# Kernel tuning notes

Hardware: AMD Instinct MI355X
Metric: run time of the kernel (lower is better)

## Reference

```python
import math
import jax, jax.numpy as jnp
import numpy as np

H = 4  # num heads
D = 512
MLP = 1024
EPS = 1e-6


def _ln(x, g, b):
    m = x.mean(-1, keepdims=True)
    v = ((x - m) ** 2).mean(-1, keepdims=True)
    return (x - m) / jnp.sqrt(v + EPS) * g + b


def _heads(x):
    B, S, d = x.shape
    return x.reshape(B, S, H, d // H).transpose(0, 2, 1, 3)  # [B,H,S,hd]


def _att(q, k, v, Wo, bo):
    # q,k,v: [B,S,D] already projected
    hd = q.shape[-1] // H
    qh, kh, vh = _heads(q), _heads(k), _heads(v)
    scores = jnp.einsum('bhqd,bhkd->bhqk', qh, kh) / math.sqrt(hd)
    probs = jax.nn.softmax(scores, axis=-1)
    ctx = jnp.einsum('bhqk,bhkd->bhqd', probs, vh)
    B, _, S, _ = ctx.shape
    ctx = ctx.transpose(0, 2, 1, 3).reshape(B, S, H * hd)
    return ctx @ Wo + bo


def setup_inputs() -> dict:
    key = jax.random.key(0)
    ks = jax.random.split(key, 32)
    i = iter(range(32))
    def w(shape, scale=0.02):
        return jax.random.normal(ks[next(i)], shape, dtype=jnp.float32) * scale
    inp = {
        'x1': jax.random.normal(ks[next(i)], (16, 1024, D), dtype=jnp.float32),
        'x2': jax.random.normal(ks[next(i)], (16, 1024, D), dtype=jnp.float32),
        'ln1_g': jnp.ones((D,), jnp.float32), 'ln1_b': jnp.zeros((D,), jnp.float32),
        'ln2_g': jnp.ones((D,), jnp.float32), 'ln2_b': jnp.zeros((D,), jnp.float32),
        'lnf_g': jnp.ones((D,), jnp.float32), 'lnf_b': jnp.zeros((D,), jnp.float32),
    }
    for name in ['q1', 'k1', 'v1', 'q2', 'k2', 'v2', 'q12', 'k12', 'v12', 'o']:
        inp['W' + name] = w((D, D))
        inp['b' + name] = jnp.zeros((D,), jnp.float32)
    inp['W1'] = w((D, MLP)); inp['b1'] = jnp.zeros((MLP,), jnp.float32)
    inp['W2'] = w((MLP, D)); inp['b2'] = jnp.zeros((D,), jnp.float32)
    return inp


def reference(x1, x2, ln1_g, ln1_b, ln2_g, ln2_b, lnf_g, lnf_b,
              Wq1, bq1, Wk1, bk1, Wv1, bv1,
              Wq2, bq2, Wk2, bk2, Wv2, bv2,
              Wq12, bq12, Wk12, bk12, Wv12, bv12,
              Wo, bo, W1, b1, W2, b2):
    identity = x1
    x1n = _ln(x1, ln1_g, ln1_b)
    x2n = _ln(x2, ln2_g, ln2_b)
    # stream-1 self-attention with residual onto normalized input
    src1 = x1n + _att(x1n @ Wq1 + bq1, x1n @ Wk1 + bk1, x1n @ Wv1 + bv1, Wo, bo)
    # stream-2 self-attention
    src2 = x2n + _att(x2n @ Wq2 + bq2, x2n @ Wk2 + bk2, x2n @ Wv2 + bv2, Wo, bo)
    # cross attention: query from src1, key/value from src2
    attn_out = _att(src1 @ Wq12 + bq12, src2 @ Wk12 + bk12, src2 @ Wv12 + bv12, Wo, bo)
    x = attn_out + identity
    h = _ln(x, lnf_g, lnf_b)
    h = jax.nn.gelu(h @ W1 + b1, approximate=False) @ W2 + b2
    return x + h
```

## Files before the change

### kernel.cpp

```cpp
#include <hip/hip_runtime.h>
#include <math.h>


#define SEQ   1024
#define DM    512
#define HDIM  128
#define MTOK  16384
#define MLPD  1024
#define SC2   ((float)(0.08838834764831845 * 1.4426950408889634))

typedef short bf16x8 __attribute__((ext_vector_type(8)));
typedef float f32x4  __attribute__((ext_vector_type(4)));
typedef float f32x16 __attribute__((ext_vector_type(16)));
typedef unsigned short us4 __attribute__((ext_vector_type(4)));

typedef unsigned int u32g __attribute__((address_space(1)));
typedef unsigned int u32l __attribute__((address_space(3)));

static __device__ __forceinline__ unsigned short f2b(float f) {
  union { float f; unsigned u; } v; v.f = f;
  unsigned r = v.u + 0x7FFFu + ((v.u >> 16) & 1u);
  return (unsigned short)(r >> 16);
}
static __device__ __forceinline__ float b2f(unsigned short h) {
  union { unsigned u; float f; } v; v.u = ((unsigned)h) << 16;
  return v.f;
}
static __device__ __forceinline__ unsigned pk2t(float a, float b) {
  union { float f; unsigned u; } va, vb; va.f = a; vb.f = b;
  return __builtin_amdgcn_perm(vb.u, va.u, 0x07060302u);
}
static __device__ __forceinline__ float ex2(float x) {
  float r; asm("v_exp_f32 %0, %1" : "=v"(r) : "v"(x)); return r;
}
static __device__ __forceinline__ void gl_lds16(const void* g, void* l) {
  __builtin_amdgcn_global_load_lds((u32g*)g, (u32l*)l, 16, 0, 0);
}

struct P12 { const float* p[12]; };
struct P9  { const float* p[9]; };

__global__ __launch_bounds__(256) void prep_kernel(P12 ws, P9 bs,
                                                   unsigned short* __restrict__ WT0,
                                                   unsigned short* __restrict__ W1t,
                                                   unsigned short* __restrict__ W2t,
                                                   float* __restrict__ bcc) {
  int bid = blockIdx.x;
  if (bid >= 3584) {
    int i = (bid - 3584) * 256 + threadIdx.x;
    if (i < 4608) bcc[i] = bs.p[i >> 9][i & 511];
    return;
  }
  __shared__ float t[32][33];
  const float* W; unsigned short* Wt; int K, N, tt;
  if (bid < 2560)      { int wi = bid >> 8; W = ws.p[wi]; Wt = WT0 + (size_t)wi * 262144; K = 512; N = 512; tt = bid & 255; }
  else if (bid < 3072) { W = ws.p[10]; Wt = W1t; K = 512;  N = 1024; tt = bid - 2560; }
  else                 { W = ws.p[11]; Wt = W2t; K = 1024; N = 512;  tt = bid - 3072; }
  int ntiles = N >> 5;
  int bx = tt % ntiles, by = tt / ntiles;
  int n0 = bx * 32, k0 = by * 32;
  int tx = threadIdx.x & 31, ty = threadIdx.x >> 5;
#pragma unroll
  for (int i = 0; i < 32; i += 8)
    t[ty + i][tx] = W[(size_t)(k0 + ty + i) * N + n0 + tx];
  __syncthreads();
#pragma unroll
  for (int i = 0; i < 32; i += 8)
    Wt[(size_t)(n0 + ty + i) * K + k0 + tx] = f2b(t[tx][ty + i]);
}

__global__ __launch_bounds__(256) void ln_kernel(const float* __restrict__ X0,
                                                 const float* __restrict__ X1,
                                                 const float* __restrict__ g0w,
                                                 const float* __restrict__ b0w,
                                                 const float* __restrict__ g1w,
                                                 const float* __restrict__ b1w,
                                                 unsigned short* __restrict__ out0,
                                                 unsigned short* __restrict__ out1) {
  int idx  = blockIdx.x * 4 + (threadIdx.x >> 6);
  int sel  = idx >> 14;
  int row  = idx & 16383;
  const float* X = sel ? X1 : X0;
  const float* gw = sel ? g1w : g0w;
  const float* bw = sel ? b1w : b0w;
  unsigned short* outB = sel ? out1 : out0;
  int lane = threadIdx.x & 63;
  const float4* xr = (const float4*)(X + (size_t)row * DM);
  float4 a = xr[lane];
  float4 c = xr[lane + 64];
  float s  = a.x + a.y + a.z + a.w + c.x + c.y + c.z + c.w;
  float s2 = a.x*a.x + a.y*a.y + a.z*a.z + a.w*a.w
           + c.x*c.x + c.y*c.y + c.z*c.z + c.w*c.w;
#pragma unroll
  for (int off = 1; off < 64; off <<= 1) {
    s  += __shfl_xor(s,  off, 64);
    s2 += __shfl_xor(s2, off, 64);
  }
  float mean = s * (1.0f / 512.0f);
  float var  = s2 * (1.0f / 512.0f) - mean * mean;
  float rstd = rsqrtf(var + 1e-6f);
  const float4* gv = (const float4*)gw;
  const float4* bv = (const float4*)bw;
  float4 g1 = gv[lane], g2 = gv[lane + 64];
  float4 b1 = bv[lane], b2 = bv[lane + 64];
  us4 o1, o2;
  o1.x = f2b((a.x - mean) * rstd * g1.x + b1.x);
  o1.y = f2b((a.y - mean) * rstd * g1.y + b1.y);
  o1.z = f2b((a.z - mean) * rstd * g1.z + b1.z);
  o1.w = f2b((a.w - mean) * rstd * g1.w + b1.w);
  o2.x = f2b((c.x - mean) * rstd * g2.x + b2.x);
  o2.y = f2b((c.y - mean) * rstd * g2.y + b2.y);
  o2.z = f2b((c.z - mean) * rstd * g2.z + b2.z);
  o2.w = f2b((c.w - mean) * rstd * g2.w + b2.w);
  *(us4*)(outB + (size_t)row * DM + lane * 4)        = o1;
  *(us4*)(outB + (size_t)row * DM + (lane + 64) * 4) = o2;
}

template <int RES, bool GELU_ACT, int OMODE>
__global__ __launch_bounds__(256, 2) void gemm_kernel(const unsigned short* __restrict__ A,
                                                      const unsigned short* __restrict__ A1,
                                                      const unsigned short* __restrict__ Bt,
                                                      const float* __restrict__ bias,
                                                      const void* __restrict__ res,
                                                      float* __restrict__ outF,
                                                      unsigned short* __restrict__ outB,
                                                      unsigned short* __restrict__ outV,
                                                      int M, int N, int K) {
  int nT = N >> 7;
  int mT = M >> 7;
  int xcd = blockIdx.x & 7;
  int idx = blockIdx.x >> 3;
  int mPerX = mT >> 3;
  int q = idx / nT;
  int tm = xcd * mPerX + q;
  int tn = idx - q * nT;
  int m0 = tm << 7, n0 = tn << 7;
  int tid = threadIdx.x, lane = tid & 63, w = tid >> 6;
  int m16 = lane & 15, q4 = lane >> 4;
  int wr = (w & 1) << 6, wc = (w >> 1) << 6;
  __shared__ unsigned short Alds[2][128 * 64];
  __shared__ unsigned short Blds[2][128 * 64];
  f32x4 acc[4][4] = {};

  const unsigned short* Aeff = A;
  const unsigned short* Bteff = Bt;
  const float* biaseff = bias;
  if (OMODE == 3) {
    int half = tm >> 7;
    Bteff = Bt + (size_t)half * 3 * 262144;
    biaseff = bias + half * 1536;
  }
  if (OMODE == 4) {
    if (tn >= 4) Aeff = A1;
  }

  int srow = lane >> 3;
  int scol = ((lane & 7) ^ srow) << 3;
  const unsigned short* Ag = Aeff  + (size_t)(m0 + w * 8 + srow) * K + scol;
  const unsigned short* Bg = Bteff + (size_t)(n0 + w * 8 + srow) * K + scol;
  int ldst = w * 512;

#pragma unroll
  for (int it = 0; it < 4; ++it) {
    gl_lds16(Ag + (size_t)it * 32 * K, Alds[0] + it * 2048 + ldst);
    gl_lds16(Bg + (size_t)it * 32 * K, Blds[0] + it * 2048 + ldst);
  }

  int nk = K >> 6;
  for (int ks = 0; ks < nk; ++ks) {
    int cur = ks & 1, nxt = cur ^ 1;
    __syncthreads();
    if (ks + 1 < nk) {
      int k0n = (ks + 1) << 6;
#pragma unroll
      for (int it = 0; it < 4; ++it) {
        gl_lds16(Ag + (size_t)it * 32 * K + k0n, Alds[nxt] + it * 2048 + ldst);
        gl_lds16(Bg + (size_t)it * 32 * K + k0n, Blds[nxt] + it * 2048 + ldst);
      }
    }
    const unsigned short* Ar = Alds[cur];
    const unsigned short* Br = Blds[cur];
#pragma unroll
    for (int kk = 0; kk < 64; kk += 32) {
      bf16x8 af[4], bfr[4];
#pragma unroll
      for (int i = 0; i < 4; ++i) {
        int row = wr + i * 16 + m16;
        af[i] = *(const bf16x8*)(Ar + row * 64 + ((((kk >> 3) + q4) ^ (m16 & 7)) << 3));
      }
#pragma unroll
      for (int j = 0; j < 4; ++j) {
        int row = wc + j * 16 + m16;
        bfr[j] = *(const bf16x8*)(Br + row * 64 + ((((kk >> 3) + q4) ^ (m16 & 7)) << 3));
      }
#pragma unroll
      for (int i = 0; i < 4; ++i)
#pragma unroll
        for (int j = 0; j < 4; ++j)
          acc[i][j] = __builtin_amdgcn_mfma_f32_16x16x32_bf16(af[i], bfr[j], acc[i][j], 0, 0, 0);
    }
  }
  if (OMODE == 3 || OMODE == 4) {
    if (n0 < 1024) {
      int stride = (OMODE == 3) ? 1024 : 512;
      unsigned short* ob = outB;
      int coff = 0;
      if (OMODE == 4 && n0 >= 512) { ob = outB + (size_t)MTOK * 512; coff = 512; }
      float sc = (n0 < 512) ? SC2 : 1.0f;
#pragma unroll
      for (int i = 0; i < 4; ++i) {
#pragma unroll
        for (int r = 0; r < 4; ++r) {
          int row = m0 + wr + i * 16 + q4 * 4 + r;
#pragma unroll
          for (int j = 0; j < 4; ++j) {
            int col = n0 + wc + j * 16 + m16;
            ob[(size_t)row * stride + col - coff] = f2b((acc[i][j][r] + biaseff[col]) * sc);
          }
        }
      }
    } else {
#pragma unroll
      for (int i = 0; i < 4; ++i) {
        int row0 = m0 + wr + i * 16 + q4 * 4;
        int s = row0 & 1023, bl = row0 >> 10;
        s = (s & ~12) | ((s & 4) << 1) | ((s & 8) >> 1);
#pragma unroll
        for (int j = 0; j < 4; ++j) {
          int col = n0 + wc + j * 16 + m16;
          int hh = (col - 1024) >> 7, hd = col & 127;
          float bb = biaseff[col];
          us4 pkv;
          pkv.x = f2b(acc[i][j][0] + bb);
          pkv.y = f2b(acc[i][j][1] + bb);
          pkv.z = f2b(acc[i][j][2] + bb);
          pkv.w = f2b(acc[i][j][3] + bb);
          *(us4*)(outV + (((size_t)(bl * 4 + hh)) * HDIM + hd) * SEQ + s) = pkv;
        }
      }
    }
  } else {
#pragma unroll
    for (int i = 0; i < 4; ++i) {
#pragma unroll
      for (int r = 0; r < 4; ++r) {
        int row = m0 + wr + i * 16 + q4 * 4 + r;
#pragma unroll
        for (int j = 0; j < 4; ++j) {
          int col = n0 + wc + j * 16 + m16;
          float v = acc[i][j][r] + bias[col];
          if (RES == 1) v += ((const float*)res)[(size_t)row * N + col];
          if (RES == 2) v += b2f(((const unsigned short*)res)[(size_t)row * N + col]);
          if (GELU_ACT) v = 0.5f * v * (1.0f + erff(v * 0.70710678118654752f));
          if (OMODE == 1) outF[(size_t)row * N + col] = v;
          else            outB[(size_t)row * N + col] = f2b(v);
        }
      }
    }
  }
}

__global__ __launch_bounds__(256, 2) void attn_kernel(const unsigned short* __restrict__ Qb_,
                                                      const unsigned short* __restrict__ Kb_,
                                                      int tstride,
                                                      const unsigned short* __restrict__ Vt,
                                                      unsigned short* __restrict__ CTX,
                                                      int pairs_per_xcd) {
  int xcd = blockIdx.x & 7;
  int i   = blockIdx.x >> 3;
  int pair = xcd * pairs_per_xcd + (i >> 3);
  int qt   = i & 7;
  int b = pair >> 2, h = pair & 3;
  int tid = threadIdx.x, lane = tid & 63, w = tid >> 6;
  int m32 = lane & 31, hf = lane >> 5;
  size_t qkoff = ((size_t)b * SEQ) * tstride + h * HDIM;
  const unsigned short* Qg = Qb_ + qkoff;
  const unsigned short* Kg = Kb_ + qkoff;
  const unsigned short* Vp = Vt + (size_t)pair * HDIM * SEQ;

  __shared__ unsigned short Klds[2][64 * 128];
  __shared__ unsigned short Vlds[2][128 * 64];

  int qrow0 = qt * 128 + w * 32;
  bf16x8 qf[8];
  {
    const unsigned short* qp = Qg + (size_t)(qrow0 + m32) * tstride + hf * 8;
#pragma unroll
    for (int ks = 0; ks < 8; ++ks) qf[ks] = *(const bf16x8*)(qp + ks * 16);
  }
  bf16x8 onesf;
#pragma unroll
  for (int j = 0; j < 8; ++j) onesf[j] = (short)0x3F80;

  const unsigned short* kp0 = Kg + (size_t)(16 * w + (lane >> 4)) * tstride
                              + (((lane & 15) ^ (lane >> 4)) << 3);
  const unsigned short* kp1 = Kg + (size_t)(16 * w + 4 + (lane >> 4)) * tstride
                              + (((lane & 15) ^ ((lane >> 4) + 4)) << 3);
  const unsigned short* vp0 = Vp + (size_t)(32 * w + (lane >> 3)) * SEQ
                              + (((lane & 7) ^ (lane >> 3)) << 3);
  int klo = 16 * w * 128;
  int vlo = 32 * w * 64;

  auto stage = [&](unsigned short* Kb, unsigned short* Vb) {
    gl_lds16(kp0,               Kb + klo);
    gl_lds16(kp1,               Kb + klo + 4 * 128);
    gl_lds16(kp0 + 8 * tstride, Kb + klo + 8 * 128);
    gl_lds16(kp1 + 8 * tstride, Kb + klo + 12 * 128);
    gl_lds16(vp0,               Vb + vlo);
    gl_lds16(vp0 + 8 * SEQ,     Vb + vlo + 8 * 64);
    gl_lds16(vp0 + 16 * SEQ,    Vb + vlo + 16 * 64);
    gl_lds16(vp0 + 24 * SEQ,    Vb + vlo + 24 * 64);
  };
  auto adv = [&]() { kp0 += 64 * tstride; kp1 += 64 * tstride; vp0 += 64; };

  f32x16 o0 = {}, o1 = {}, o2 = {}, o3 = {};
  f32x16 lacc = {};
  bf16x8 pa0, pa1, pa2, pa3;
  bf16x8 pb0, pb1, pb2, pb3;

  auto qk = [&](const unsigned short* Kr, f32x16& s0, f32x16& s1) {
#pragma unroll
    for (int ks = 0; ks < 8; ++ks) {
      int ch = 2 * ks + hf;
      bf16x8 kf0 = *(const bf16x8*)(Kr + m32 * 128 + ((ch ^ (m32 & 7)) << 3));
      s0 = __builtin_amdgcn_mfma_f32_32x32x16_bf16(kf0, qf[ks], s0, 0, 0, 0);
      int k1r = 32 + m32;
      bf16x8 kf1 = *(const bf16x8*)(Kr + k1r * 128 + ((ch ^ (k1r & 7)) << 3));
      s1 = __builtin_amdgcn_mfma_f32_32x32x16_bf16(kf1, qf[ks], s1, 0, 0, 0);
    }
  };
  auto mkpa = [&](const f32x16& s0, const f32x16& s1,
                  bf16x8& q0, bf16x8& q1, bf16x8& q2, bf16x8& q3) {
    union { unsigned u[4]; bf16x8 v; } uu;
#pragma unroll
    for (int g = 0; g < 2; ++g) {
      uu.u[0] = pk2t(ex2(s0[8*g+0]), ex2(s0[8*g+1]));
      uu.u[1] = pk2t(ex2(s0[8*g+2]), ex2(s0[8*g+3]));
      uu.u[2] = pk2t(ex2(s0[8*g+4]), ex2(s0[8*g+5]));
      uu.u[3] = pk2t(ex2(s0[8*g+6]), ex2(s0[8*g+7]));
      if (g == 0) q0 = uu.v; else q1 = uu.v;
    }
#pragma unroll
    for (int g = 0; g < 2; ++g) {
      uu.u[0] = pk2t(ex2(s1[8*g+0]), ex2(s1[8*g+1]));
      uu.u[1] = pk2t(ex2(s1[8*g+2]), ex2(s1[8*g+3]));
      uu.u[2] = pk2t(ex2(s1[8*g+4]), ex2(s1[8*g+5]));
      uu.u[3] = pk2t(ex2(s1[8*g+6]), ex2(s1[8*g+7]));
      if (g == 0) q2 = uu.v; else q3 = uu.v;
    }
  };
  auto pv = [&](const unsigned short* Vr,
                const bf16x8& q0, const bf16x8& q1, const bf16x8& q2, const bf16x8& q3) {
#pragma unroll
    for (int ks = 0; ks < 4; ++ks) {
      const bf16x8& pk = (ks == 0) ? q0 : (ks == 1) ? q1 : (ks == 2) ? q2 : q3;
      int ch = 2 * ks + hf;
      int sw = m32 & 7;
      lacc = __builtin_amdgcn_mfma_f32_32x32x16_bf16(pk, onesf, lacc, 0, 0, 0);
      {
        bf16x8 vf = *(const bf16x8*)(Vr + m32 * 64 + ((ch ^ sw) << 3));
        o0 = __builtin_amdgcn_mfma_f32_32x32x16_bf16(pk, vf, o0, 0, 0, 0);
      }
      {
        bf16x8 vf = *(const bf16x8*)(Vr + (32 + m32) * 64 + ((ch ^ sw) << 3));
        o1 = __builtin_amdgcn_mfma_f32_32x32x16_bf16(pk, vf, o1, 0, 0, 0);
      }
      {
        bf16x8 vf = *(const bf16x8*)(Vr + (64 + m32) * 64 + ((ch ^ sw) << 3));
        o2 = __builtin_amdgcn_mfma_f32_32x32x16_bf16(pk, vf, o2, 0, 0, 0);
      }
      {
        bf16x8 vf = *(const bf16x8*)(Vr + (96 + m32) * 64 + ((ch ^ sw) << 3));
        o3 = __builtin_amdgcn_mfma_f32_32x32x16_bf16(pk, vf, o3, 0, 0, 0);
      }
    }
  };

  stage(Klds[0], Vlds[0]);
  __syncthreads();
  adv();
  stage(Klds[1], Vlds[1]);
  {
    f32x16 s0 = {}, s1 = {};
    qk(Klds[0], s0, s1);
    mkpa(s0, s1, pa0, pa1, pa2, pa3);
  }

  for (int t = 0; t < 15; ++t) {
    int cur = t & 1, nxt = cur ^ 1;
    __syncthreads();
    f32x16 s0 = {}, s1 = {};
    qk(Klds[nxt], s0, s1);
    pv(Vlds[cur], pa0, pa1, pa2, pa3);
    mkpa(s0, s1, pb0, pb1, pb2, pb3);
    __syncthreads();
    if (t < 14) { adv(); stage(Klds[cur], Vlds[cur]); }
    pa0 = pb0; pa1 = pb1; pa2 = pb2; pa3 = pb3;
  }
  pv(Vlds[1], pa0, pa1, pa2, pa3);

  size_t obase = ((size_t)b * SEQ + qrow0) * DM + h * HDIM;
#pragma unroll
  for (int g = 0; g < 4; ++g) {
#pragma unroll
    for (int r = 0; r < 4; ++r) {
      int reg = 4 * g + r;
      int rowl = 8 * g + 4 * hf + r;
      float inv = 1.0f / lacc[reg];
      size_t off = obase + (size_t)rowl * DM + m32;
      CTX[off]      = f2b(o0[reg] * inv);
      CTX[off + 32] = f2b(o1[reg] * inv);
      CTX[off + 64] = f2b(o2[reg] * inv);
      CTX[off + 96] = f2b(o3[reg] * inv);
    }
  }
}

extern "C" void kernel_launch(void* const* d_in, const int* in_sizes, int n_in,
                              void* d_out, int out_size, void* d_ws, size_t ws_size,
                              hipStream_t stream) {
  const float* x1    = (const float*)d_in[0];
  const float* x2    = (const float*)d_in[1];
  const float* ln1_g = (const float*)d_in[2];
  const float* ln1_b = (const float*)d_in[3];
  const float* ln2_g = (const float*)d_in[4];
  const float* ln2_b = (const float*)d_in[5];
  const float* lnf_g = (const float*)d_in[6];
  const float* lnf_b = (const float*)d_in[7];
  P12 wsrc;
  for (int i = 0; i < 10; ++i) wsrc.p[i] = (const float*)d_in[8 + 2 * i];
  wsrc.p[10] = (const float*)d_in[28];
  wsrc.p[11] = (const float*)d_in[30];
  P9 bsrc;
  for (int i = 0; i < 9; ++i) bsrc.p[i] = (const float*)d_in[9 + 2 * i];
  const float* bo   = (const float*)d_in[27];
  const float* b1   = (const float*)d_in[29];
  const float* b2   = (const float*)d_in[31];

  char* ws = (char*)d_ws;
  size_t off = 0;
  auto alloc = [&](size_t bytes) -> char* {
    char* p = ws + off;
    off += (bytes + 255) & ~(size_t)255;
    return p;
  };
  unsigned short* WT0 = (unsigned short*)alloc((size_t)10 * 512 * 512 * 2);
  auto WT = [&](int i) { return WT0 + (size_t)i * 262144; };
  unsigned short* W1t = (unsigned short*)alloc((size_t)1024 * 512 * 2);
  unsigned short* W2t = (unsigned short*)alloc((size_t)512 * 1024 * 2);
  float*          bcc = (float*)alloc(4608 * 4);
  unsigned short* XN  = (unsigned short*)alloc((size_t)2 * MTOK * DM * 2);
  unsigned short* QKb = (unsigned short*)alloc((size_t)2 * MTOK * 1024 * 2);
  unsigned short* Vtb = (unsigned short*)alloc((size_t)128 * HDIM * SEQ * 2);
  unsigned short* CT  = (unsigned short*)alloc((size_t)2 * MTOK * DM * 2);
  float*          Xf  = (float*)alloc((size_t)MTOK * DM * 4);
  unsigned short* XN1 = XN + (size_t)MTOK * DM;
  unsigned short* MID = QKb;
  unsigned short* HN  = Vtb;
  float* bias_self  = bcc;
  float* bias_cross = bcc + 3072;

  prep_kernel<<<3602, 256, 0, stream>>>(wsrc, bsrc, WT0, W1t, W2t, bcc);

  ln_kernel<<<2 * MTOK / 4, 256, 0, stream>>>(x1, x2, ln1_g, ln1_b, ln2_g, ln2_b, XN, XN1);

  gemm_kernel<0, false, 3><<<3072, 256, 0, stream>>>(XN, nullptr, WT0, bias_self,
      nullptr, nullptr, QKb, Vtb, 32768, 1536, 512);

  attn_kernel<<<128 * 8, 256, 0, stream>>>(QKb, QKb + 512, 1024, Vtb, CT, 16);

  gemm_kernel<2, false, 0><<<1024, 256, 0, stream>>>(CT, nullptr, WT(9), bo, XN,
      nullptr, XN, nullptr, 32768, 512, 512);

  gemm_kernel<0, false, 4><<<1536, 256, 0, stream>>>(XN, XN1, WT(6), bias_cross,
      nullptr, nullptr, QKb, Vtb, 16384, 1536, 512);

  attn_kernel<<<64 * 8, 256, 0, stream>>>(QKb, QKb + (size_t)MTOK * 512, 512, Vtb, CT, 8);

  gemm_kernel<1, false, 1><<<512, 256, 0, stream>>>(CT, nullptr, WT(9), bo, x1,
      Xf, nullptr, nullptr, 16384, 512, 512);

  ln_kernel<<<MTOK / 4, 256, 0, stream>>>(Xf, Xf, lnf_g, lnf_b, lnf_g, lnf_b, HN, HN);

  gemm_kernel<0, true,  0><<<1024, 256, 0, stream>>>(HN, nullptr, W1t, b1,
      nullptr, nullptr, MID, nullptr, 16384, 1024, 512);
  gemm_kernel<1, false, 1><<<512, 256, 0, stream>>>(MID, nullptr, W2t, b2,
      Xf, (float*)d_out, nullptr, nullptr, 16384, 512, 1024);
}
```

Measured before the change: 506.5 us.

## Switch GEMM tiles to 256x128 with K-step 32 and new LDS swizzle

The GEMM kernel now computes a 256x128 output tile per block instead of 128x128, with each wave owning 128x64 and accumulating into 8x4 MFMA fragments. The K step drops from 64 to 32, the LDS staging layout and XOR swizzle are redesigned for 32-wide rows, and all launch grids are halved. The aim is more reuse of B tiles and fewer blocks per GEMM. The cost is more accumulator registers per thread under launch_bounds(256,2), twice as many barriers per K, and fewer blocks to fill the CUs.

New measurement: 559.6 us. 1.1x slower.

```diff
diff --git a/kernel.cpp b/kernel.cpp
--- a/kernel.cpp
+++ b/kernel.cpp
@@ -127,26 +127,26 @@
                                                       unsigned short* __restrict__ outV,
                                                       int M, int N, int K) {
   int nT = N >> 7;
-  int mT = M >> 7;
+  int mT = M >> 8;
   int xcd = blockIdx.x & 7;
   int idx = blockIdx.x >> 3;
   int mPerX = mT >> 3;
   int q = idx / nT;
   int tm = xcd * mPerX + q;
   int tn = idx - q * nT;
-  int m0 = tm << 7, n0 = tn << 7;
+  int m0 = tm << 8, n0 = tn << 7;
   int tid = threadIdx.x, lane = tid & 63, w = tid >> 6;
   int m16 = lane & 15, q4 = lane >> 4;
-  int wr = (w & 1) << 6, wc = (w >> 1) << 6;
-  __shared__ unsigned short Alds[2][128 * 64];
-  __shared__ unsigned short Blds[2][128 * 64];
-  f32x4 acc[4][4] = {};
+  int wr = (w & 1) << 7, wc = (w >> 1) << 6;
+  __shared__ unsigned short Alds[2][256 * 32];
+  __shared__ unsigned short Blds[2][128 * 32];
+  f32x4 acc[8][4] = {};
 
   const unsigned short* Aeff = A;
   const unsigned short* Bteff = Bt;
   const float* biaseff = bias;
   if (OMODE == 3) {
-    int half = tm >> 7;
+    int half = tm >> 6;
     Bteff = Bt + (size_t)half * 3 * 262144;
     biaseff = bias + half * 1536;
   }
@@ -154,51 +154,49 @@
     if (tn >= 4) Aeff = A1;
   }
 
-  int srow = lane >> 3;
-  int scol = ((lane & 7) ^ srow) << 3;
-  const unsigned short* Ag = Aeff  + (size_t)(m0 + w * 8 + srow) * K + scol;
-  const unsigned short* Bg = Bteff + (size_t)(n0 + w * 8 + srow) * K + scol;
-  int ldst = w * 512;
-
-#pragma unroll
-  for (int it = 0; it < 4; ++it) {
-    gl_lds16(Ag + (size_t)it * 32 * K, Alds[0] + it * 2048 + ldst);
-    gl_lds16(Bg + (size_t)it * 32 * K, Blds[0] + it * 2048 + ldst);
-  }
-
-  int nk = K >> 6;
+  int r4   = lane >> 2;
+  int swz  = (r4 ^ (r4 >> 2)) & 3;
+  int scol = ((lane & 3) ^ swz) << 3;
+  const unsigned short* Ag = Aeff  + (size_t)(m0 + w * 64 + r4) * K + scol;
+  const unsigned short* Bg = Bteff + (size_t)(n0 + w * 32 + r4) * K + scol;
+
+#pragma unroll
+  for (int it = 0; it < 4; ++it)
+    gl_lds16(Ag + (size_t)it * 16 * K, Alds[0] + w * 2048 + it * 512);
+#pragma unroll
+  for (int it = 0; it < 2; ++it)
+    gl_lds16(Bg + (size_t)it * 16 * K, Blds[0] + w * 1024 + it * 512);
+
+  int rsw  = (m16 ^ (m16 >> 2)) & 3;
+  int roff = (q4 ^ rsw) << 3;
+
+  int nk = K >> 5;
   for (int ks = 0; ks < nk; ++ks) {
     int cur = ks & 1, nxt = cur ^ 1;
     __syncthreads();
     if (ks + 1 < nk) {
-      int k0n = (ks + 1) << 6;
-#pragma unroll
-      for (int it = 0; it < 4; ++it) {
-        gl_lds16(Ag + (size_t)it * 32 * K + k0n, Alds[nxt] + it * 2048 + ldst);
-        gl_lds16(Bg + (size_t)it * 32 * K + k0n, Blds[nxt] + it * 2048 + ldst);
-      }
+      int k0n = (ks + 1) << 5;
+#pragma unroll
+      for (int it = 0; it < 4; ++it)
+        gl_lds16(Ag + (size_t)it * 16 * K + k0n, Alds[nxt] + w * 2048 + it * 512);
+#pragma unroll
+      for (int it = 0; it < 2; ++it)
+        gl_lds16(Bg + (size_t)it * 16 * K + k0n, Blds[nxt] + w * 1024 + it * 512);
     }
     const unsigned short* Ar = Alds[cur];
     const unsigned short* Br = Blds[cur];
-#pragma unroll
-    for (int kk = 0; kk < 64; kk += 32) {
-      bf16x8 af[4], bfr[4];
-#pragma unroll
-      for (int i = 0; i < 4; ++i) {
-        int row = wr + i * 16 + m16;
-        af[i] = *(const bf16x8*)(Ar + row * 64 + ((((kk >> 3) + q4) ^ (m16 & 7)) << 3));
-      }
-#pragma unroll
-      for (int j = 0; j < 4; ++j) {
-        int row = wc + j * 16 + m16;
-        bfr[j] = *(const bf16x8*)(Br + row * 64 + ((((kk >> 3) + q4) ^ (m16 & 7)) << 3));
-      }
-#pragma unroll
-      for (int i = 0; i < 4; ++i)
-#pragma unroll
-        for (int j = 0; j < 4; ++j)
-          acc[i][j] = __builtin_amdgcn_mfma_f32_16x16x32_bf16(af[i], bfr[j], acc[i][j], 0, 0, 0);
-    }
+    bf16x8 af[8], bfr[4];
+#pragma unroll
+    for (int i = 0; i < 8; ++i)
+      af[i] = *(const bf16x8*)(Ar + (wr + i * 16 + m16) * 32 + roff);
+#pragma unroll
+    for (int j = 0; j < 4; ++j)
+      bfr[j] = *(const bf16x8*)(Br + (wc + j * 16 + m16) * 32 + roff);
+#pragma unroll
+    for (int i = 0; i < 8; ++i)
+#pragma unroll
+      for (int j = 0; j < 4; ++j)
+        acc[i][j] = __builtin_amdgcn_mfma_f32_16x16x32_bf16(af[i], bfr[j], acc[i][j], 0, 0, 0);
   }
   if (OMODE == 3 || OMODE == 4) {
     if (n0 < 1024) {
@@ -208,7 +206,7 @@
       if (OMODE == 4 && n0 >= 512) { ob = outB + (size_t)MTOK * 512; coff = 512; }
       float sc = (n0 < 512) ? SC2 : 1.0f;
 #pragma unroll
-      for (int i = 0; i < 4; ++i) {
+      for (int i = 0; i < 8; ++i) {
 #pragma unroll
         for (int r = 0; r < 4; ++r) {
           int row = m0 + wr + i * 16 + q4 * 4 + r;
@@ -221,7 +219,7 @@
       }
     } else {
 #pragma unroll
-      for (int i = 0; i < 4; ++i) {
+      for (int i = 0; i < 8; ++i) {
         int row0 = m0 + wr + i * 16 + q4 * 4;
         int s = row0 & 1023, bl = row0 >> 10;
         s = (s & ~12) | ((s & 4) << 1) | ((s & 8) >> 1);
@@ -241,7 +239,7 @@
     }
   } else {
 #pragma unroll
-    for (int i = 0; i < 4; ++i) {
+    for (int i = 0; i < 8; ++i) {
 #pragma unroll
       for (int r = 0; r < 4; ++r) {
         int row = m0 + wr + i * 16 + q4 * 4 + r;
@@ -464,26 +462,26 @@
 
   ln_kernel<<<2 * MTOK / 4, 256, 0, stream>>>(x1, x2, ln1_g, ln1_b, ln2_g, ln2_b, XN, XN1);
 
-  gemm_kernel<0, false, 3><<<3072, 256, 0, stream>>>(XN, nullptr, WT0, bias_self,
+  gemm_kernel<0, false, 3><<<1536, 256, 0, stream>>>(XN, nullptr, WT0, bias_self,
       nullptr, nullptr, QKb, Vtb, 32768, 1536, 512);
 
   attn_kernel<<<128 * 8, 256, 0, stream>>>(QKb, QKb + 512, 1024, Vtb, CT, 16);
 
-  gemm_kernel<2, false, 0><<<1024, 256, 0, stream>>>(CT, nullptr, WT(9), bo, XN,
+  gemm_kernel<2, false, 0><<<512, 256, 0, stream>>>(CT, nullptr, WT(9), bo, XN,
       nullptr, XN, nullptr, 32768, 512, 512);
 
-  gemm_kernel<0, false, 4><<<1536, 256, 0, stream>>>(XN, XN1, WT(6), bias_cross,
+  gemm_kernel<0, false, 4><<<768, 256, 0, stream>>>(XN, XN1, WT(6), bias_cross,
       nullptr, nullptr, QKb, Vtb, 16384, 1536, 512);
 
   attn_kernel<<<64 * 8, 256, 0, stream>>>(QKb, QKb + (size_t)MTOK * 512, 512, Vtb, CT, 8);
 
-  gemm_kernel<1, false, 1><<<512, 256, 0, stream>>>(CT, nullptr, WT(9), bo, x1,
+  gemm_kernel<1, false, 1><<<256, 256, 0, stream>>>(CT, nullptr, WT(9), bo, x1,
       Xf, nullptr, nullptr, 16384, 512, 512);
 
   ln_kernel<<<MTOK / 4, 256, 0, stream>>>(Xf, Xf, lnf_g, lnf_b, lnf_g, lnf_b, HN, HN);
 
-  gemm_kernel<0, true,  0><<<1024, 256, 0, stream>>>(HN, nullptr, W1t, b1,
+  gemm_kernel<0, true,  0><<<512, 256, 0, stream>>>(HN, nullptr, W1t, b1,
       nullptr, nullptr, MID, nullptr, 16384, 1024, 512);
-  gemm_kernel<1, false, 1><<<512, 256, 0, stream>>>(MID, nullptr, W2t, b2,
+  gemm_kernel<1, false, 1><<<256, 256, 0, stream>>>(MID, nullptr, W2t, b2,
       Xf, (float*)d_out, nullptr, nullptr, 16384, 512, 1024);
 }
```
